# Kernel optimization log

Hardware: AMD Instinct MI355X
Metric: run time of the kernel (lower is better)

Reference implementation:

```python
import jax, jax.numpy as jnp
import numpy as np

# dims: batch, spatial H x W, channels-last
B, H, W = 16, 256, 256
CIN, COUT = 32, 32
N_MODES = (32, 32)
EM0 = N_MODES[0] // 2        # 16 (eff modes along first spatial dim)
EM1 = N_MODES[1] // 2 + 1    # 17 (eff modes along last rfft dim)
WF = W // 2 + 1              # 129 rfft bins


def setup_inputs() -> dict:
    key = jax.random.key(0)
    kx, k1r, k1i, k2r, k2i, kb = jax.random.split(key, 6)
    wshape = (CIN, COUT, EM0, EM1)
    # variance-scaling-ish scale: scale=0.5, fan_avg
    wscale = np.float32(np.sqrt(0.5 / ((CIN + COUT) / 2.0)))
    return {
        "x": jax.random.normal(kx, (B, H, W, CIN), dtype=jnp.float32),
        "w1_real": jax.random.normal(k1r, wshape, dtype=jnp.float32) * wscale,
        "w1_imag": jax.random.normal(k1i, wshape, dtype=jnp.float32) * wscale,
        "w2_real": jax.random.normal(k2r, wshape, dtype=jnp.float32) * wscale,
        "w2_imag": jax.random.normal(k2i, wshape, dtype=jnp.float32) * wscale,
        "bias": jax.random.normal(kb, (1, 1, 1, COUT), dtype=jnp.float32) * 0.1,
    }


def reference(x, w1_real, w1_imag, w2_real, w2_imag, bias):
    # forward-normalized real FFT over the two spatial axes: (B,H,WF,CIN) complex64
    x_ft = jnp.fft.rfftn(x, axes=(1, 2), norm="forward")
    w1 = w1_real + 1j * w1_imag  # corner signs=(+1,): low rows
    w2 = w2_real + 1j * w2_imag  # corner signs=(-1,): high (negative-freq) rows
    # per-corner complex mode mixing: contract input channels -> output channels
    top = jnp.einsum("bhwi,iohw->bhwo", x_ft[:, :EM0, :EM1, :], w1)
    bot = jnp.einsum("bhwi,iohw->bhwo", x_ft[:, -EM0:, :EM1, :], w2)
    out_ft = jnp.zeros((B, H, WF, COUT), dtype=jnp.complex64)
    out_ft = out_ft.at[:, :EM0, :EM1, :].set(top)
    out_ft = out_ft.at[:, -EM0:, :EM1, :].set(bot)
    y = jnp.fft.irfftn(out_ft, s=(H, W), axes=(1, 2), norm="forward")
    return y + bias
```

## Files before the change

kernel.cpp:

```cpp
#include <hip/hip_runtime.h>

#define NB 16
#define NH 256
#define EM1 17
#define TWO_PI 6.283185307179586f

typedef short short8 __attribute__((ext_vector_type(8)));
typedef float floatx4 __attribute__((ext_vector_type(4)));

__device__ __forceinline__ unsigned f2b(float x){ union{float f; unsigned u;} v; v.f=x; return v.u; }
__device__ __forceinline__ float b2f(unsigned u){ union{float f; unsigned u;} v; v.u=u; return v.f; }

__device__ __forceinline__ void cmul_upd(float& tr, float& ti, float wr, float wi) {
    float nr = tr * wr - ti * wi;
    float ni = tr * wi + ti * wr;
    tr = nr; ti = ni;
}

__global__ __launch_bounds__(256, 2) void k1_fwdW_mfma(const float* __restrict__ x,
                                                       float* __restrict__ Xw) {
    __shared__ __align__(16) short alds[16384];
    const int t = threadIdx.x;
    const int w = t >> 6;
    const int l = t & 63;
    const int mt = w & 1;
    const int g  = w >> 1;
    const int nn = (g == 0) ? 2 : 1;

    short8 Bh[2][8], Bl[2][8];
    const float sc = 1.0f / 65536.0f;
    #pragma unroll
    for (int u = 0; u < 2; ++u) {
        const int nt  = (g == 0) ? u : 2;
        const int n   = nt * 16 + (l & 15);
        const int kwv = n >> 1;
        const int par = n & 1;
        const bool live = (u < nn) && (n < 34);
        const float dth = (TWO_PI / 256.f) * (float)kwv;
        #pragma unroll
        for (int ks = 0; ks < 8; ++ks) {
            const int k0 = ks * 32 + (l >> 4) * 8;
            float s, c; sincosf(dth * (float)k0, &s, &c);
            float sd, cd; sincosf(dth, &sd, &cd);
            short8 vh, vl;
            #pragma unroll
            for (int j = 0; j < 8; ++j) {
                float v = live ? ((par ? -s : c) * sc) : 0.f;
                unsigned ub = f2b(v);
                short h16 = (short)(ub >> 16);
                float rres = v - b2f(ub & 0xFFFF0000u);
                short l16 = (short)(f2b(rres) >> 16);
                vh[j] = h16; vl[j] = l16;
                float ncv = c * cd - s * sd, nsv = c * sd + s * cd;
                c = ncv; s = nsv;
            }
            Bh[u][ks] = vh; Bl[u][ks] = vl;
        }
    }

    const int i   = t & 31;
    const int slot = t >> 5;
    const int i15 = i & 15, imt = i >> 4;
    const int i15l = l & 15, ql = l >> 4;

    for (int ir = 0; ir < 8; ++ir) {
        const int row = blockIdx.x * 8 + ir;
        const int b = row >> 8, y = row & 255;
        __syncthreads();
        {
            const float* rp = x + (size_t)row * 8192;
            unsigned* al32 = (unsigned*)alds;
            #pragma unroll
            for (int c = 0; c < 16; ++c) {
                const int xp = slot + (c << 3);
                float v0 = rp[xp * 64 + i];
                float v1 = rp[xp * 64 + 32 + i];
                unsigned u0 = f2b(v0), u1 = f2b(v1);
                unsigned hi = (u0 >> 16) | (u1 & 0xFFFF0000u);
                float r0 = v0 - b2f(u0 & 0xFFFF0000u);
                float r1 = v1 - b2f(u1 & 0xFFFF0000u);
                unsigned lo = (f2b(r0) >> 16) | (f2b(r1) & 0xFFFF0000u);
                const int ks = xp >> 4, q = (xp & 15) >> 2, dw = xp & 3;
                const int base = (ks * 2 + imt) * 256 + (q * 16 + i15) * 4 + dw;
                al32[base] = hi;
                al32[base + 16 * 256] = lo;
            }
        }
        __syncthreads();
        floatx4 acc0 = {0.f, 0.f, 0.f, 0.f};
        floatx4 acc1 = {0.f, 0.f, 0.f, 0.f};
        #pragma unroll
        for (int ks = 0; ks < 8; ++ks) {
            const short8 ah = *(const short8*)(alds + ((ks * 2 + mt) * 512) + l * 8);
            const short8 al = *(const short8*)(alds + ((16 + ks * 2 + mt) * 512) + l * 8);
            acc0 = __builtin_amdgcn_mfma_f32_16x16x32_bf16(ah, Bh[0][ks], acc0, 0, 0, 0);
            acc0 = __builtin_amdgcn_mfma_f32_16x16x32_bf16(ah, Bl[0][ks], acc0, 0, 0, 0);
            acc0 = __builtin_amdgcn_mfma_f32_16x16x32_bf16(al, Bh[0][ks], acc0, 0, 0, 0);
            if (nn == 2) {
                acc1 = __builtin_amdgcn_mfma_f32_16x16x32_bf16(ah, Bh[1][ks], acc1, 0, 0, 0);
                acc1 = __builtin_amdgcn_mfma_f32_16x16x32_bf16(ah, Bl[1][ks], acc1, 0, 0, 0);
                acc1 = __builtin_amdgcn_mfma_f32_16x16x32_bf16(al, Bh[1][ks], acc1, 0, 0, 0);
            }
        }
        #pragma unroll
        for (int u = 0; u < 2; ++u) {
            if (u >= nn) break;
            const int nt = (g == 0) ? u : 2;
            const int n = nt * 16 + i15l;
            if (n < 34) {
                const int kwv = n >> 1, par = n & 1;
                float* dst = Xw + (((size_t)(b * 17 + kwv) * 256 + y) * 64) + par;
                const floatx4 a = (u == 0) ? acc0 : acc1;
                #pragma unroll
                for (int r = 0; r < 4; ++r) {
                    const int ii = mt * 16 + ql * 4 + r;
                    dst[ii * 2] = a[r];
                }
            }
        }
    }
}

__global__ __launch_bounds__(256) void k2_fwdH(const float2* __restrict__ Xw,
                                               float2* __restrict__ xft) {
    __shared__ __align__(16) float2 xsh[256 * 16];
    const int t = threadIdx.x;
    const int bk = blockIdx.x;
    const int b = bk / 34;
    const int rem = bk - b * 34;
    const int kw = rem >> 1, ih = rem & 1;
    const float2* src = Xw + ((size_t)(b * 17 + kw) * 256) * 32 + ih * 16;
    #pragma unroll
    for (int q = 0; q < 8; ++q) {
        int v = q * 256 + t;
        int yy = v >> 3, quad = v & 7;
        ((float4*)xsh)[v] = *(const float4*)(src + (size_t)yy * 32 + quad * 2);
    }
    __syncthreads();
    const int m = t & 31, ip = t >> 5;
    const int kh = (m < 16) ? m : m - 32;
    float wc, ws; sincosf(-TWO_PI * (float)kh * (1.f / 256.f), &ws, &wc);
    float tr = 1.f, ti = 0.f;
    float a0r = 0.f, a0i = 0.f, a1r = 0.f, a1i = 0.f;
    const float* xp = (const float*)xsh + ip * 4;
    #pragma unroll 8
    for (int yy = 0; yy < 256; ++yy) {
        float4 v = *(const float4*)(xp + yy * 32);
        a0r = fmaf(v.x, tr, a0r); a0r = fmaf(-v.y, ti, a0r);
        a0i = fmaf(v.x, ti, a0i); a0i = fmaf(v.y, tr, a0i);
        a1r = fmaf(v.z, tr, a1r); a1r = fmaf(-v.w, ti, a1r);
        a1i = fmaf(v.z, ti, a1i); a1i = fmaf(v.w, tr, a1i);
        cmul_upd(tr, ti, wc, ws);
    }
    size_t o = ((size_t)b * 32 + m) * 544 + (size_t)kw * 32 + ih * 16 + ip * 2;
    *(float4*)(xft + o) = make_float4(a0r, a0i, a1r, a1i);
}

__global__ __launch_bounds__(256) void k3_mix(const float2* __restrict__ xft,
                                              const float* __restrict__ w1r,
                                              const float* __restrict__ w1i,
                                              const float* __restrict__ w2r,
                                              const float* __restrict__ w2i,
                                              float2* __restrict__ oft) {
    __shared__ float wrl[1024];
    __shared__ float wil[1024];
    __shared__ float2 xbl[512];
    int bk = blockIdx.x;
    int m = bk / 17, kw = bk - m * 17;
    const float* wr_g; const float* wi_g; int h;
    if (m < 16) { wr_g = w1r; wi_g = w1i; h = m; }
    else        { wr_g = w2r; wi_g = w2i; h = m - 16; }
    int t = threadIdx.x;
#pragma unroll
    for (int c = 0; c < 4; ++c) {
        int u = (c << 8) + t;
        int ii = u >> 5, o = u & 31;
        size_t gi = ((size_t)(ii * 32 + o) * 16 + h) * 17 + kw;
        wrl[u] = wr_g[gi]; wil[u] = wi_g[gi];
    }
#pragma unroll
    for (int c = 0; c < 2; ++c) {
        int u = (c << 8) + t;
        int bb = u >> 5, ii = u & 31;
        xbl[u] = xft[(size_t)bb * 17408 + (size_t)m * 544 + (size_t)kw * 32 + ii];
    }
    __syncthreads();
    int o = t & 31, bg = t >> 5;
#pragma unroll
    for (int rr = 0; rr < 2; ++rr) {
        int bb = bg + 8 * rr;
        float ar = 0.f, ai = 0.f;
#pragma unroll
        for (int ii = 0; ii < 32; ++ii) {
            float2 xv = xbl[bb * 32 + ii];
            float wr_ = wrl[ii * 32 + o], wi_ = wil[ii * 32 + o];
            ar = fmaf(xv.x, wr_, ar); ar = fmaf(-xv.y, wi_, ar);
            ai = fmaf(xv.x, wi_, ai); ai = fmaf(xv.y, wr_, ai);
        }
        oft[(size_t)bb * 17408 + (size_t)m * 544 + (size_t)kw * 32 + o] =
            make_float2(ar, ai);
    }
}

__global__ __launch_bounds__(256) void k4_invH(const float2* __restrict__ oft,
                                               float2* __restrict__ T) {
    __shared__ __align__(16) float2 ol[32 * 16];
    const int t = threadIdx.x;
    const int bk = blockIdx.x;
    const int b = bk / 34;
    const int rem = bk - b * 34;
    const int kw = rem >> 1, oh = rem & 1;
    {
        int mm = t >> 3, quad = t & 7;
        ((float4*)ol)[t] = *(const float4*)(oft + (size_t)b * 17408 +
                                            (size_t)mm * 544 + (size_t)kw * 32 + oh * 16 + quad * 2);
    }
    __syncthreads();
    const int y = t;
    float uc, us; sincosf(TWO_PI * (float)y * (1.f / 256.f), &us, &uc);
    float tr = 1.f, ti = 0.f;
    float ar[16], ai[16];
    #pragma unroll
    for (int o = 0; o < 16; ++o) { ar[o] = 0.f; ai[o] = 0.f; }
    for (int m = 0; m < 32; ++m) {
        if (m == 16) ti = -ti;
        #pragma unroll
        for (int o2 = 0; o2 < 8; ++o2) {
            float4 v = *(const float4*)((const float*)ol + m * 32 + o2 * 4);
            int o = o2 * 2;
            ar[o]   = fmaf(v.x, tr, ar[o]);   ar[o]   = fmaf(-v.y, ti, ar[o]);
            ai[o]   = fmaf(v.x, ti, ai[o]);   ai[o]   = fmaf(v.y, tr, ai[o]);
            ar[o+1] = fmaf(v.z, tr, ar[o+1]); ar[o+1] = fmaf(-v.w, ti, ar[o+1]);
            ai[o+1] = fmaf(v.z, ti, ai[o+1]); ai[o+1] = fmaf(v.w, tr, ai[o+1]);
        }
        cmul_upd(tr, ti, uc, us);
    }
    float2* dst = T + ((size_t)(b * 256 + y) * 17 + kw) * 32 + oh * 16;
    #pragma unroll
    for (int o2 = 0; o2 < 8; ++o2) {
        *(float4*)(dst + o2 * 2) =
            make_float4(ar[o2*2], ai[o2*2], ar[o2*2+1], ai[o2*2+1]);
    }
}

__global__ __launch_bounds__(256) void k5_invW(const float2* __restrict__ T,
                                               const float* __restrict__ bias,
                                               float* __restrict__ out) {
    __shared__ __align__(16) float2 tl[544];
    __shared__ float bl[32];
    const int t = threadIdx.x;
    const int blk = blockIdx.x;
    const float4* src4 = (const float4*)(T + (size_t)blk * 544);
    for (int u = t; u < 272; u += 256) ((float4*)tl)[u] = src4[u];
    if (t < 32) bl[t] = bias[t];
    __syncthreads();
    const int o8 = t & 3, xq = t >> 2;
    float c0, s0; sincosf(TWO_PI * (float)(xq * 4) * (1.f / 256.f), &s0, &c0);
    const float CC = 0.99969881869620422f, SS = 0.02454122852291229f;
    float ur[4], ui[4];
    ur[0] = c0; ui[0] = s0;
    #pragma unroll
    for (int k = 1; k < 4; ++k) {
        ur[k] = ur[k-1] * CC - ui[k-1] * SS;
        ui[k] = ur[k-1] * SS + ui[k-1] * CC;
    }
    float tr_[4], ti_[4];
    #pragma unroll
    for (int k = 0; k < 4; ++k) { tr_[k] = ur[k]; ti_[k] = ui[k]; }
    float acc[4][8];
    #pragma unroll
    for (int k = 0; k < 4; ++k)
        #pragma unroll
        for (int o = 0; o < 8; ++o) acc[k][o] = 0.f;
    #pragma unroll 4
    for (int kw = 1; kw < 17; ++kw) {
        #pragma unroll
        for (int o2 = 0; o2 < 4; ++o2) {
            float4 v = *(const float4*)((const float*)tl + kw * 64 + o8 * 16 + o2 * 4);
            #pragma unroll
            for (int k = 0; k < 4; ++k) {
                acc[k][o2*2]   = fmaf(v.x, tr_[k], acc[k][o2*2]);
                acc[k][o2*2]   = fmaf(-v.y, ti_[k], acc[k][o2*2]);
                acc[k][o2*2+1] = fmaf(v.z, tr_[k], acc[k][o2*2+1]);
                acc[k][o2*2+1] = fmaf(-v.w, ti_[k], acc[k][o2*2+1]);
            }
        }
        #pragma unroll
        for (int k = 0; k < 4; ++k) cmul_upd(tr_[k], ti_[k], ur[k], ui[k]);
    }
    float base[8];
    #pragma unroll
    for (int o = 0; o < 8; ++o) {
        int og = o8 * 8 + o;
        base[o] = tl[og].x + bl[og];
    }
    float* orow = out + (size_t)blk * 8192;
    #pragma unroll
    for (int k = 0; k < 4; ++k) {
        int xx = xq * 4 + k;
        float res[8];
        #pragma unroll
        for (int o = 0; o < 8; ++o) res[o] = fmaf(2.f, acc[k][o], base[o]);
        float* dst = orow + xx * 32 + o8 * 8;
        *(float4*)(dst)     = make_float4(res[0], res[1], res[2], res[3]);
        *(float4*)(dst + 4) = make_float4(res[4], res[5], res[6], res[7]);
    }
}

extern "C" void kernel_launch(void* const* d_in, const int* in_sizes, int n_in,
                              void* d_out, int out_size, void* d_ws, size_t ws_size,
                              hipStream_t stream) {
    const float* x    = (const float*)d_in[0];
    const float* w1r  = (const float*)d_in[1];
    const float* w1i  = (const float*)d_in[2];
    const float* w2r  = (const float*)d_in[3];
    const float* w2i  = (const float*)d_in[4];
    const float* bias = (const float*)d_in[5];
    float* out = (float*)d_out;

    char* ws = (char*)d_ws;
    float2* Xw  = (float2*)ws;
    float2* T   = Xw;
    float2* xft = (float2*)(ws + 17825792);
    float2* oft = (float2*)(ws + 17825792 + 2228224);

    k1_fwdW_mfma<<<512, 256, 0, stream>>>(x, (float*)Xw);
    k2_fwdH<<<NB * EM1 * 2, 256, 0, stream>>>(Xw, xft);
    k3_mix <<<32 * EM1, 256, 0, stream>>>(xft, w1r, w1i, w2r, w2i, oft);
    k4_invH<<<NB * EM1 * 2, 256, 0, stream>>>(oft, T);
    k5_invW<<<NB * NH, 256, 0, stream>>>(T, bias, out);
}
```

Baseline: 315.9 us.

## Fuse forward H-DFT, channel mixing and inverse H-DFT into one kernel

Replaces the three middle kernels (forward DFT along H, complex channel mixing, inverse DFT along H) with a single 512-thread kernel per (batch, kw). Intermediate spectra stay in shared memory instead of round-tripping through global memory. A new pre-kernel transposes the weights into an interleaved complex layout indexed by (kw, mode, in, out) so the fused mixing step can read float4s. In exchange the grid is halved to 272 blocks of 512 threads, which may lower occupancy and parallelism, and T no longer aliases Xw, so the workspace grows.

```diff
diff --git a/kernel.cpp b/kernel.cpp
--- a/kernel.cpp
+++ b/kernel.cpp
@@ -15,6 +15,35 @@
     float nr = tr * wr - ti * wi;
     float ni = tr * wi + ti * wr;
     tr = nr; ti = ni;
+}
+
+__global__ __launch_bounds__(256) void k0_wt(const float* __restrict__ w1r,
+                                             const float* __restrict__ w1i,
+                                             const float* __restrict__ w2r,
+                                             const float* __restrict__ w2i,
+                                             float2* __restrict__ wt) {
+    __shared__ __align__(16) float l1r[2176], l1i[2176], l2r[2176], l2i[2176];
+    const int t = threadIdx.x;
+    const int i = blockIdx.x >> 2;
+    const int oq = blockIdx.x & 3;
+    const size_t off = (size_t)(i * 32 + oq * 8) * 272;
+    for (int u = t; u < 544; u += 256) {
+        ((float4*)l1r)[u] = ((const float4*)(w1r + off))[u];
+        ((float4*)l1i)[u] = ((const float4*)(w1i + off))[u];
+        ((float4*)l2r)[u] = ((const float4*)(w2r + off))[u];
+        ((float4*)l2i)[u] = ((const float4*)(w2i + off))[u];
+    }
+    __syncthreads();
+    for (int v = t; v < 4352; v += 256) {
+        const int kw = v >> 8;
+        const int rem = v & 255;
+        const int m = rem >> 3, o8 = rem & 7;
+        const int h = m & 15;
+        const int lidx = o8 * 272 + h * 17 + kw;
+        const float vr = (m < 16) ? l1r[lidx] : l2r[lidx];
+        const float vi = (m < 16) ? l1i[lidx] : l2i[lidx];
+        wt[((size_t)(kw * 32 + m) * 32 + i) * 32 + oq * 8 + o8] = make_float2(vr, vi);
+    }
 }
 
 __global__ __launch_bounds__(256, 2) void k1_fwdW_mfma(const float* __restrict__ x,
@@ -121,125 +150,86 @@
     }
 }
 
-__global__ __launch_bounds__(256) void k2_fwdH(const float2* __restrict__ Xw,
-                                               float2* __restrict__ xft) {
-    __shared__ __align__(16) float2 xsh[256 * 16];
+__global__ __launch_bounds__(512) void kmid(const float2* __restrict__ Xw,
+                                            const float2* __restrict__ wt,
+                                            float2* __restrict__ T) {
+    __shared__ __align__(16) float2 xsh[128 * 32];
+    __shared__ __align__(16) float2 xhat[32 * 32];
+    __shared__ __align__(16) float2 osl[32 * 32];
     const int t = threadIdx.x;
     const int bk = blockIdx.x;
-    const int b = bk / 34;
-    const int rem = bk - b * 34;
-    const int kw = rem >> 1, ih = rem & 1;
-    const float2* src = Xw + ((size_t)(b * 17 + kw) * 256) * 32 + ih * 16;
-    #pragma unroll
-    for (int q = 0; q < 8; ++q) {
-        int v = q * 256 + t;
-        int yy = v >> 3, quad = v & 7;
-        ((float4*)xsh)[v] = *(const float4*)(src + (size_t)yy * 32 + quad * 2);
-    }
-    __syncthreads();
-    const int m = t & 31, ip = t >> 5;
-    const int kh = (m < 16) ? m : m - 32;
+    const int b = bk / 17, kw = bk - b * 17;
+    const float4* src4 = (const float4*)(Xw + (size_t)bk * 8192);
+
+    const int m1 = t & 31, ip2 = t >> 5;
+    const int kh = (m1 < 16) ? m1 : m1 - 32;
     float wc, ws; sincosf(-TWO_PI * (float)kh * (1.f / 256.f), &ws, &wc);
     float tr = 1.f, ti = 0.f;
     float a0r = 0.f, a0i = 0.f, a1r = 0.f, a1i = 0.f;
-    const float* xp = (const float*)xsh + ip * 4;
-    #pragma unroll 8
-    for (int yy = 0; yy < 256; ++yy) {
-        float4 v = *(const float4*)(xp + yy * 32);
-        a0r = fmaf(v.x, tr, a0r); a0r = fmaf(-v.y, ti, a0r);
-        a0i = fmaf(v.x, ti, a0i); a0i = fmaf(v.y, tr, a0i);
-        a1r = fmaf(v.z, tr, a1r); a1r = fmaf(-v.w, ti, a1r);
-        a1i = fmaf(v.z, ti, a1i); a1i = fmaf(v.w, tr, a1i);
-        cmul_upd(tr, ti, wc, ws);
-    }
-    size_t o = ((size_t)b * 32 + m) * 544 + (size_t)kw * 32 + ih * 16 + ip * 2;
-    *(float4*)(xft + o) = make_float4(a0r, a0i, a1r, a1i);
-}
-
-__global__ __launch_bounds__(256) void k3_mix(const float2* __restrict__ xft,
-                                              const float* __restrict__ w1r,
-                                              const float* __restrict__ w1i,
-                                              const float* __restrict__ w2r,
-                                              const float* __restrict__ w2i,
-                                              float2* __restrict__ oft) {
-    __shared__ float wrl[1024];
-    __shared__ float wil[1024];
-    __shared__ float2 xbl[512];
-    int bk = blockIdx.x;
-    int m = bk / 17, kw = bk - m * 17;
-    const float* wr_g; const float* wi_g; int h;
-    if (m < 16) { wr_g = w1r; wi_g = w1i; h = m; }
-    else        { wr_g = w2r; wi_g = w2i; h = m - 16; }
-    int t = threadIdx.x;
-#pragma unroll
-    for (int c = 0; c < 4; ++c) {
-        int u = (c << 8) + t;
-        int ii = u >> 5, o = u & 31;
-        size_t gi = ((size_t)(ii * 32 + o) * 16 + h) * 17 + kw;
-        wrl[u] = wr_g[gi]; wil[u] = wi_g[gi];
-    }
-#pragma unroll
-    for (int c = 0; c < 2; ++c) {
-        int u = (c << 8) + t;
-        int bb = u >> 5, ii = u & 31;
-        xbl[u] = xft[(size_t)bb * 17408 + (size_t)m * 544 + (size_t)kw * 32 + ii];
-    }
+    const float* xp = (const float*)xsh + ip2 * 4;
+    for (int half = 0; half < 2; ++half) {
+        __syncthreads();
+        #pragma unroll
+        for (int q = 0; q < 4; ++q) {
+            int v = q * 512 + t;
+            ((float4*)xsh)[v] = src4[half * 2048 + v];
+        }
+        __syncthreads();
+        #pragma unroll 8
+        for (int yy = 0; yy < 128; ++yy) {
+            float4 v = *(const float4*)(xp + yy * 64);
+            a0r = fmaf(v.x, tr, a0r); a0r = fmaf(-v.y, ti, a0r);
+            a0i = fmaf(v.x, ti, a0i); a0i = fmaf(v.y, tr, a0i);
+            a1r = fmaf(v.z, tr, a1r); a1r = fmaf(-v.w, ti, a1r);
+            a1i = fmaf(v.z, ti, a1i); a1i = fmaf(v.w, tr, a1i);
+            cmul_upd(tr, ti, wc, ws);
+        }
+    }
+    *(float4*)(xhat + m1 * 32 + ip2 * 2) = make_float4(a0r, a0i, a1r, a1i);
     __syncthreads();
-    int o = t & 31, bg = t >> 5;
-#pragma unroll
-    for (int rr = 0; rr < 2; ++rr) {
-        int bb = bg + 8 * rr;
-        float ar = 0.f, ai = 0.f;
-#pragma unroll
+
+    {
+        const int o2 = t & 15, m = t >> 4;
+        const float4* wp = (const float4*)wt + ((size_t)(kw * 32 + m) * 32) * 16 + o2;
+        float ar0 = 0.f, ai0 = 0.f, ar1 = 0.f, ai1 = 0.f;
+        #pragma unroll 8
         for (int ii = 0; ii < 32; ++ii) {
-            float2 xv = xbl[bb * 32 + ii];
-            float wr_ = wrl[ii * 32 + o], wi_ = wil[ii * 32 + o];
-            ar = fmaf(xv.x, wr_, ar); ar = fmaf(-xv.y, wi_, ar);
-            ai = fmaf(xv.x, wi_, ai); ai = fmaf(xv.y, wr_, ai);
-        }
-        oft[(size_t)bb * 17408 + (size_t)m * 544 + (size_t)kw * 32 + o] =
-            make_float2(ar, ai);
-    }
-}
-
-__global__ __launch_bounds__(256) void k4_invH(const float2* __restrict__ oft,
-                                               float2* __restrict__ T) {
-    __shared__ __align__(16) float2 ol[32 * 16];
-    const int t = threadIdx.x;
-    const int bk = blockIdx.x;
-    const int b = bk / 34;
-    const int rem = bk - b * 34;
-    const int kw = rem >> 1, oh = rem & 1;
+            float2 xv = xhat[m * 32 + ii];
+            float4 wv = wp[(size_t)ii * 16];
+            ar0 = fmaf(xv.x, wv.x, ar0); ar0 = fmaf(-xv.y, wv.y, ar0);
+            ai0 = fmaf(xv.x, wv.y, ai0); ai0 = fmaf(xv.y, wv.x, ai0);
+            ar1 = fmaf(xv.x, wv.z, ar1); ar1 = fmaf(-xv.y, wv.w, ar1);
+            ai1 = fmaf(xv.x, wv.w, ai1); ai1 = fmaf(xv.y, wv.z, ai1);
+        }
+        *(float4*)(osl + m * 32 + o2 * 2) = make_float4(ar0, ai0, ar1, ai1);
+    }
+    __syncthreads();
+
     {
-        int mm = t >> 3, quad = t & 7;
-        ((float4*)ol)[t] = *(const float4*)(oft + (size_t)b * 17408 +
-                                            (size_t)mm * 544 + (size_t)kw * 32 + oh * 16 + quad * 2);
-    }
-    __syncthreads();
-    const int y = t;
-    float uc, us; sincosf(TWO_PI * (float)y * (1.f / 256.f), &us, &uc);
-    float tr = 1.f, ti = 0.f;
-    float ar[16], ai[16];
-    #pragma unroll
-    for (int o = 0; o < 16; ++o) { ar[o] = 0.f; ai[o] = 0.f; }
-    for (int m = 0; m < 32; ++m) {
-        if (m == 16) ti = -ti;
-        #pragma unroll
-        for (int o2 = 0; o2 < 8; ++o2) {
-            float4 v = *(const float4*)((const float*)ol + m * 32 + o2 * 4);
-            int o = o2 * 2;
-            ar[o]   = fmaf(v.x, tr, ar[o]);   ar[o]   = fmaf(-v.y, ti, ar[o]);
-            ai[o]   = fmaf(v.x, ti, ai[o]);   ai[o]   = fmaf(v.y, tr, ai[o]);
-            ar[o+1] = fmaf(v.z, tr, ar[o+1]); ar[o+1] = fmaf(-v.w, ti, ar[o+1]);
-            ai[o+1] = fmaf(v.z, ti, ai[o+1]); ai[o+1] = fmaf(v.w, tr, ai[o+1]);
-        }
-        cmul_upd(tr, ti, uc, us);
-    }
-    float2* dst = T + ((size_t)(b * 256 + y) * 17 + kw) * 32 + oh * 16;
-    #pragma unroll
-    for (int o2 = 0; o2 < 8; ++o2) {
-        *(float4*)(dst + o2 * 2) =
-            make_float4(ar[o2*2], ai[o2*2], ar[o2*2+1], ai[o2*2+1]);
+        const int y = t & 255, oh = t >> 8;
+        float uc, us; sincosf(TWO_PI * (float)y * (1.f / 256.f), &us, &uc);
+        float tr2 = 1.f, ti2 = 0.f;
+        float ar[16], ai[16];
+        #pragma unroll
+        for (int o = 0; o < 16; ++o) { ar[o] = 0.f; ai[o] = 0.f; }
+        for (int m = 0; m < 32; ++m) {
+            if (m == 16) ti2 = -ti2;
+            #pragma unroll
+            for (int o2 = 0; o2 < 8; ++o2) {
+                float4 v = *(const float4*)((const float*)osl + m * 64 + oh * 32 + o2 * 4);
+                int o = o2 * 2;
+                ar[o]   = fmaf(v.x, tr2, ar[o]);   ar[o]   = fmaf(-v.y, ti2, ar[o]);
+                ai[o]   = fmaf(v.x, ti2, ai[o]);   ai[o]   = fmaf(v.y, tr2, ai[o]);
+                ar[o+1] = fmaf(v.z, tr2, ar[o+1]); ar[o+1] = fmaf(-v.w, ti2, ar[o+1]);
+                ai[o+1] = fmaf(v.z, ti2, ai[o+1]); ai[o+1] = fmaf(v.w, tr2, ai[o+1]);
+            }
+            cmul_upd(tr2, ti2, uc, us);
+        }
+        float2* dst = T + ((size_t)(b * 256 + y) * 17 + kw) * 32 + oh * 16;
+        #pragma unroll
+        for (int o2 = 0; o2 < 8; ++o2)
+            *(float4*)(dst + o2 * 2) =
+                make_float4(ar[o2*2], ai[o2*2], ar[o2*2+1], ai[o2*2+1]);
     }
 }
 
@@ -319,14 +309,12 @@
     float* out = (float*)d_out;
 
     char* ws = (char*)d_ws;
-    float2* Xw  = (float2*)ws;
-    float2* T   = Xw;
-    float2* xft = (float2*)(ws + 17825792);
-    float2* oft = (float2*)(ws + 17825792 + 2228224);
-
+    float2* Xw = (float2*)ws;
+    float2* T  = (float2*)(ws + 17825792);
+    float2* wt = (float2*)(ws + 2 * 17825792);
+
+    k0_wt<<<128, 256, 0, stream>>>(w1r, w1i, w2r, w2i, wt);
     k1_fwdW_mfma<<<512, 256, 0, stream>>>(x, (float*)Xw);
-    k2_fwdH<<<NB * EM1 * 2, 256, 0, stream>>>(Xw, xft);
-    k3_mix <<<32 * EM1, 256, 0, stream>>>(xft, w1r, w1i, w2r, w2i, oft);
-    k4_invH<<<NB * EM1 * 2, 256, 0, stream>>>(oft, T);
+    kmid<<<NB * EM1, 512, 0, stream>>>(Xw, wt, T);
     k5_invW<<<NB * NH, 256, 0, stream>>>(T, bias, out);
 }
```

New measurement: 318.7 us. Within noise of the previous version (+0.9%).
